# Kernel optimization log

Measured on AMD Instinct MI355X. Metric: run time of the kernel, lower is better.

The kernel has to match this reference:

```python
import jax, jax.numpy as jnp
import numpy as np

N = 50000
EPS = 1e-5


def gcn_conv(x, edge_index, W, b):
    # x: [N, Fin] -> [N, Fout]; symmetric-normalized aggregation with self-loops
    h = x @ W  # [N, Fout]
    src = jnp.concatenate([edge_index[0], jnp.arange(N, dtype=edge_index.dtype)])
    dst = jnp.concatenate([edge_index[1], jnp.arange(N, dtype=edge_index.dtype)])
    deg = jax.ops.segment_sum(jnp.ones_like(dst, dtype=h.dtype), dst, num_segments=N)
    dinv = jnp.where(deg > 0, jax.lax.rsqrt(deg), 0.0)
    norm = dinv[src] * dinv[dst]  # [E+N]
    msg = h[src] * norm[:, None]  # [E+N, Fout]
    out = jax.ops.segment_sum(msg, dst, num_segments=N)
    return out + b


def batch_norm_eval(x, gamma, beta, mean, var):
    return (x - mean) * jax.lax.rsqrt(var + EPS) * gamma + beta


def setup_inputs() -> dict:
    key = jax.random.key(0)
    ks = jax.random.split(key, 16)
    Fin, H, C = 128, 64, 40
    inp = {
        "x": jax.random.normal(ks[0], (N, Fin), dtype=jnp.float32),
        "edge_index": jax.random.randint(ks[1], (2, 1600000), 0, N, dtype=jnp.int64),
        "W1": jax.random.normal(ks[2], (Fin, H), dtype=jnp.float32) / np.sqrt(Fin),
        "b1": jnp.zeros((H,), jnp.float32),
        "g1": jax.random.normal(ks[3], (H,), jnp.float32) * 0.1 + 1.0,
        "be1": jax.random.normal(ks[4], (H,), jnp.float32) * 0.1,
        "m1": jax.random.normal(ks[5], (H,), jnp.float32) * 0.1,
        "v1": jax.random.uniform(ks[6], (H,), jnp.float32, 0.5, 1.5),
        "W2": jax.random.normal(ks[7], (H, H), dtype=jnp.float32) / np.sqrt(H),
        "b2": jnp.zeros((H,), jnp.float32),
        "g2": jax.random.normal(ks[8], (H,), jnp.float32) * 0.1 + 1.0,
        "be2": jax.random.normal(ks[9], (H,), jnp.float32) * 0.1,
        "m2": jax.random.normal(ks[10], (H,), jnp.float32) * 0.1,
        "v2": jax.random.uniform(ks[11], (H,), jnp.float32, 0.5, 1.5),
        "W3": jax.random.normal(ks[12], (H, C), dtype=jnp.float32) / np.sqrt(H),
        "b3": jnp.zeros((C,), jnp.float32),
    }
    return inp


def reference(x, edge_index, W1, b1, g1, be1, m1, v1, W2, b2, g2, be2, m2, v2, W3, b3):
    # eval-mode forward: dropout is identity, BatchNorm uses running stats
    h = gcn_conv(x, edge_index, W1, b1)
    h = jax.nn.relu(batch_norm_eval(h, g1, be1, m1, v1))
    h = gcn_conv(h, edge_index, W2, b2)
    h = jax.nn.relu(batch_norm_eval(h, g2, be2, m2, v2))
    return gcn_conv(h, edge_index, W3, b3)
```

## Files before the change

### kernel.cpp

```cpp
#include <hip/hip_runtime.h>
#include <hip/hip_fp16.h>

#define BN_EPS 1e-5f


__global__ void k_bcount(const int* __restrict__ dst, int* __restrict__ btot, int E, int B) {
    __shared__ int cnt[256];
    int tid = threadIdx.x;
    cnt[tid] = 0;
    __syncthreads();
    int e0 = blockIdx.x * 2048;
#pragma unroll
    for (int j = 0; j < 8; ++j) {
        int e = e0 + j * 256 + tid;
        if (e < E) atomicAdd(&cnt[dst[e] >> 8], 1);
    }
    __syncthreads();
    if (tid < B && cnt[tid] > 0) atomicAdd(&btot[tid], cnt[tid]);
}

__global__ void k_bscan(const int* __restrict__ btot, int* __restrict__ bbase,
                        int* __restrict__ bcur, int* __restrict__ row_ptr, int N, int B) {
    __shared__ int sc[256];
    int tid = threadIdx.x;
    int v = (tid < B) ? btot[tid] : 0;
    sc[tid] = v;
    __syncthreads();
    for (int off = 1; off < 256; off <<= 1) {
        int t = (tid >= off) ? sc[tid - off] : 0;
        __syncthreads();
        sc[tid] += t;
        __syncthreads();
    }
    int excl = sc[tid] - v;
    if (tid < B) { bbase[tid] = excl; bcur[tid] = excl; }
    if (tid == B - 1) { bbase[B] = excl + v; row_ptr[N] = excl + v; }
}

__global__ void k_bscatter(const int* __restrict__ src, const int* __restrict__ dst,
                           int* bcur, unsigned int* __restrict__ ebuf, int E, int B) {
    __shared__ int cnt[256];
    __shared__ int gb[256];
    int tid = threadIdx.x;
    cnt[tid] = 0;
    __syncthreads();
    int e0 = blockIdx.x * 2048;
    int bk[8], rk[8];
    unsigned int pay[8];
#pragma unroll
    for (int j = 0; j < 8; ++j) {
        int e = e0 + j * 256 + tid;
        if (e < E) {
            int d = dst[e];
            int b = d >> 8;
            bk[j] = b;
            rk[j] = atomicAdd(&cnt[b], 1);
            pay[j] = (unsigned int)src[e] | ((unsigned int)(d & 255) << 16);
        } else {
            bk[j] = -1; rk[j] = 0; pay[j] = 0;
        }
    }
    __syncthreads();
    if (tid < B && cnt[tid] > 0) gb[tid] = atomicAdd(&bcur[tid], cnt[tid]);
    __syncthreads();
#pragma unroll
    for (int j = 0; j < 8; ++j)
        if (bk[j] >= 0) ebuf[gb[bk[j]] + rk[j]] = pay[j];
}

__global__ void k_bfinal(const unsigned int* __restrict__ ebuf, const int* __restrict__ bbase,
                         int* __restrict__ row_ptr, float* __restrict__ dinv,
                         unsigned short* __restrict__ col, int N) {
    __shared__ int cnt[256];
    __shared__ int sc[256];
    __shared__ int cur[256];
    int tid = threadIdx.x;
    int b = blockIdx.x;
    int node0 = b << 8;
    int ebeg = bbase[b], eend = bbase[b + 1];

    cnt[tid] = 0;
    __syncthreads();
    for (int i = ebeg + tid; i < eend; i += 256)
        atomicAdd(&cnt[ebuf[i] >> 16], 1);
    __syncthreads();
    int myc = cnt[tid];
    sc[tid] = myc;
    __syncthreads();
    for (int off = 1; off < 256; off <<= 1) {
        int t = (tid >= off) ? sc[tid - off] : 0;
        __syncthreads();
        sc[tid] += t;
        __syncthreads();
    }
    int excl = sc[tid] - myc;
    cur[tid] = ebeg + excl;
    int node = node0 + tid;
    if (node < N) {
        row_ptr[node] = ebeg + excl;
        dinv[node] = rsqrtf((float)(myc + 1));
    }
    __syncthreads();
    for (int i = ebeg + tid; i < eend; i += 256) {
        unsigned int p = ebuf[i];
        int dl = p >> 16;
        int pos = atomicAdd(&cur[dl], 1);
        col[pos] = (unsigned short)(p & 0xFFFFu);
    }
}

template <int K, int FOUT>
__launch_bounds__(256)
__global__ void k_gemm_scale(const float* __restrict__ X, const float* __restrict__ W,
                             const float* __restrict__ dinv, __half* __restrict__ HS, int N) {
    __shared__ float xs[K][65];
    __shared__ float wl[K][FOUT];
    int tid = threadIdx.x;
    int row0 = blockIdx.x * 64;

    for (int idx = tid; idx < K * FOUT; idx += 256)
        wl[idx / FOUT][idx % FOUT] = W[idx];
    for (int idx = tid; idx < 64 * K; idx += 256) {
        int r = idx / K, k = idx % K;
        int row = row0 + r;
        xs[k][r] = (row < N) ? X[row * K + k] : 0.0f;
    }
    __syncthreads();

    int tc = tid & 15, tr = tid >> 4;
    if (4 * tc < FOUT) {
        float acc[4][4] = {};
#pragma unroll 8
        for (int k = 0; k < K; ++k) {
            float a0 = xs[k][4 * tr + 0];
            float a1 = xs[k][4 * tr + 1];
            float a2 = xs[k][4 * tr + 2];
            float a3 = xs[k][4 * tr + 3];
            const float4 w = *reinterpret_cast<const float4*>(&wl[k][4 * tc]);
            acc[0][0] += a0 * w.x; acc[0][1] += a0 * w.y; acc[0][2] += a0 * w.z; acc[0][3] += a0 * w.w;
            acc[1][0] += a1 * w.x; acc[1][1] += a1 * w.y; acc[1][2] += a1 * w.z; acc[1][3] += a1 * w.w;
            acc[2][0] += a2 * w.x; acc[2][1] += a2 * w.y; acc[2][2] += a2 * w.z; acc[2][3] += a2 * w.w;
            acc[3][0] += a3 * w.x; acc[3][1] += a3 * w.y; acc[3][2] += a3 * w.z; acc[3][3] += a3 * w.w;
        }
#pragma unroll
        for (int i = 0; i < 4; ++i) {
            int row = row0 + 4 * tr + i;
            if (row < N) {
                float dv = dinv[row];
                __half2 h0 = __floats2half2_rn(dv * acc[i][0], dv * acc[i][1]);
                __half2 h1 = __floats2half2_rn(dv * acc[i][2], dv * acc[i][3]);
                __half2* p = reinterpret_cast<__half2*>(&HS[row * FOUT + 4 * tc]);
                p[0] = h0; p[1] = h1;
            }
        }
    }
}

template <int FOUT, bool BN>
__launch_bounds__(256)
__global__ void k_agg(const __half2* __restrict__ hs2, const unsigned short* __restrict__ col,
                      const int* __restrict__ row_ptr, const float* __restrict__ dinv,
                      const float* __restrict__ b, const float* __restrict__ g,
                      const float* __restrict__ be, const float* __restrict__ m,
                      const float* __restrict__ v, float* __restrict__ out, int N) {
    constexpr int NP = FOUT / 2;
    int gtid = blockIdx.x * blockDim.x + threadIdx.x;
    int wave = gtid >> 6;
    int lane = gtid & 63;
    int half = lane >> 5;
    int l = lane & 31;
    int nwaves = (gridDim.x * blockDim.x) >> 6;
    bool active = l < NP;

    float b0 = 0.f, b1 = 0.f, s0f = 0.f, s1f = 0.f, t0f = 0.f, t1f = 0.f;
    if (active) {
        b0 = b[2 * l]; b1 = b[2 * l + 1];
        if (BN) {
            s0f = g[2 * l] * rsqrtf(v[2 * l] + BN_EPS);
            s1f = g[2 * l + 1] * rsqrtf(v[2 * l + 1] + BN_EPS);
            t0f = be[2 * l] - m[2 * l] * s0f;
            t1f = be[2 * l + 1] - m[2 * l + 1] * s1f;
        }
    }

    float2* out2 = reinterpret_cast<float2*>(out);

    for (int node = wave; node < N; node += nwaves) {
        int beg = row_ptr[node], end = row_ptr[node + 1];
        float ax = 0.f, ay = 0.f, bx = 0.f, by = 0.f;
        float cx = 0.f, cy = 0.f, dx = 0.f, dy = 0.f;
        if (active && half == 0) {
            float2 t = __half22float2(hs2[node * NP + l]);
            ax = t.x; ay = t.y;
        }
        int e = beg + half;
        for (; e + 6 < end; e += 8) {
            int i0 = col[e], i1 = col[e + 2], i2 = col[e + 4], i3 = col[e + 6];
            if (active) {
                float2 t0 = __half22float2(hs2[i0 * NP + l]);
                float2 t1 = __half22float2(hs2[i1 * NP + l]);
                float2 t2 = __half22float2(hs2[i2 * NP + l]);
                float2 t3 = __half22float2(hs2[i3 * NP + l]);
                ax += t0.x; ay += t0.y;
                bx += t1.x; by += t1.y;
                cx += t2.x; cy += t2.y;
                dx += t3.x; dy += t3.y;
            }
        }
        for (; e < end; e += 2) {
            int i0 = col[e];
            if (active) {
                float2 t0 = __half22float2(hs2[i0 * NP + l]);
                ax += t0.x; ay += t0.y;
            }
        }
        float sx = (ax + bx) + (cx + dx);
        float sy = (ay + by) + (cy + dy);
        sx += __shfl_xor(sx, 32);
        sy += __shfl_xor(sy, 32);
        if (active && half == 0) {
            float dv = dinv[node];
            float o0 = dv * sx + b0;
            float o1 = dv * sy + b1;
            if (BN) {
                o0 = fmaxf(o0 * s0f + t0f, 0.0f);
                o1 = fmaxf(o1 * s1f + t1f, 0.0f);
            }
            out2[node * NP + l] = make_float2(o0, o1);
        }
    }
}


extern "C" void kernel_launch(void* const* d_in, const int* in_sizes, int n_in,
                              void* d_out, int out_size, void* d_ws, size_t ws_size,
                              hipStream_t stream) {
    const float* x   = (const float*)d_in[0];
    const int*   ei  = (const int*)d_in[1];
    const float* W1  = (const float*)d_in[2];
    const float* b1  = (const float*)d_in[3];
    const float* g1  = (const float*)d_in[4];
    const float* be1 = (const float*)d_in[5];
    const float* m1  = (const float*)d_in[6];
    const float* v1  = (const float*)d_in[7];
    const float* W2  = (const float*)d_in[8];
    const float* b2  = (const float*)d_in[9];
    const float* g2  = (const float*)d_in[10];
    const float* be2 = (const float*)d_in[11];
    const float* m2  = (const float*)d_in[12];
    const float* v2  = (const float*)d_in[13];
    const float* W3  = (const float*)d_in[14];
    const float* b3  = (const float*)d_in[15];

    const int FIN = 128, H = 64;
    int N = in_sizes[0] / FIN;
    int E = in_sizes[1] / 2;
    const int* src = ei;
    const int* dst = ei + E;
    int B = (N + 255) >> 8;

    char* ws = (char*)d_ws;
    size_t off = 0;
    auto carve = [&](size_t bytes) -> void* {
        void* p = ws + off;
        off += (bytes + 255) & ~(size_t)255;
        return p;
    };
    float*  dinv    = (float*)carve((size_t)N * 4);
    int*    row_ptr = (int*)carve((size_t)(N + 1) * 4);
    unsigned short* col = (unsigned short*)carve((size_t)E * 2);
    unsigned int*   ebuf = (unsigned int*)carve((size_t)E * 4);
    __half* hs      = (__half*)carve((size_t)N * H * 2);
    float*  y       = (float*)carve((size_t)N * H * 4);
    int*    btot    = (int*)carve(512 * 4);
    int*    bbase   = (int*)carve(512 * 4);
    int*    bcur    = (int*)carve(512 * 4);
    (void)ws_size; (void)n_in; (void)out_size;

    int eb2k = (E + 2047) / 2048;

    hipMemsetAsync(btot, 0, (size_t)B * 4, stream);
    k_bcount<<<eb2k, 256, 0, stream>>>(dst, btot, E, B);
    k_bscan<<<1, 256, 0, stream>>>(btot, bbase, bcur, row_ptr, N, B);
    k_bscatter<<<eb2k, 256, 0, stream>>>(src, dst, bcur, ebuf, E, B);
    k_bfinal<<<B, 256, 0, stream>>>(ebuf, bbase, row_ptr, dinv, col, N);

    int gb = (N + 63) / 64;
    const __half2* hs2 = (const __half2*)hs;
    k_gemm_scale<128, 64><<<gb, 256, 0, stream>>>(x, W1, dinv, hs, N);
    k_agg<64, true><<<4096, 256, 0, stream>>>(hs2, col, row_ptr, dinv, b1, g1, be1, m1, v1, y, N);
    k_gemm_scale<64, 64><<<gb, 256, 0, stream>>>(y, W2, dinv, hs, N);
    k_agg<64, true><<<4096, 256, 0, stream>>>(hs2, col, row_ptr, dinv, b2, g2, be2, m2, v2, y, N);
    k_gemm_scale<64, 40><<<gb, 256, 0, stream>>>(y, W3, dinv, hs, N);
    k_agg<40, false><<<4096, 256, 0, stream>>>(hs2, col, row_ptr, dinv, b3, nullptr, nullptr, nullptr, nullptr,
                                               (float*)d_out, N);
}
```

Measured before the change: 262.5 us.

## Use fp16 dot2 in dense transforms and store intermediate activations in fp16

The GEMM kernels now stage inputs and weights in shared memory as packed half2 values and accumulate with the packed fp16 dot-product instruction into fp32, halving the multiply-add instruction count. The BN+ReLU aggregation outputs are written as fp16, and the following GEMMs read fp16 input with 16-byte loads, halving that intermediate traffic. The cost is extra rounding of the inputs, weights and hidden activations to fp16, which can reduce accuracy relative to the fp32 reference.

```diff
diff --git a/kernel.cpp b/kernel.cpp
--- a/kernel.cpp
+++ b/kernel.cpp
@@ -2,6 +2,13 @@
 #include <hip/hip_fp16.h>
 
 #define BN_EPS 1e-5f
+
+typedef _Float16 half2_t __attribute__((ext_vector_type(2)));
+typedef _Float16 half8_t __attribute__((ext_vector_type(8)));
+
+static __device__ __forceinline__ float fdot2(half2_t a, half2_t b, float c) {
+    return __builtin_amdgcn_fdot2(a, b, c, false);
+}
 
 
 __global__ void k_bcount(const int* __restrict__ dst, int* __restrict__ btot, int E, int B) {
@@ -109,48 +116,85 @@
     }
 }
 
-template <int K, int FOUT>
+template <int K, int FOUT, bool FP16IN>
 __launch_bounds__(256)
-__global__ void k_gemm_scale(const float* __restrict__ X, const float* __restrict__ W,
-                             const float* __restrict__ dinv, __half* __restrict__ HS, int N) {
-    __shared__ float xs[K][65];
-    __shared__ float wl[K][FOUT];
+__global__ void k_gemm_scale(const void* __restrict__ Xv, const float* __restrict__ W,
+                             const float* __restrict__ dinv, half2_t* __restrict__ HS, int N) {
+    constexpr int KK = K / 2;
+    constexpr int XSTR = (K == 128) ? 66 : 36;
+    __shared__ half2_t xs2[64][XSTR];
+    __shared__ half2_t wl2[KK][FOUT];
     int tid = threadIdx.x;
     int row0 = blockIdx.x * 64;
 
-    for (int idx = tid; idx < K * FOUT; idx += 256)
-        wl[idx / FOUT][idx % FOUT] = W[idx];
-    for (int idx = tid; idx < 64 * K; idx += 256) {
-        int r = idx / K, k = idx % K;
-        int row = row0 + r;
-        xs[k][r] = (row < N) ? X[row * K + k] : 0.0f;
+    if constexpr (FP16IN) {
+        const _Float16* X = (const _Float16*)Xv;
+        constexpr int U = 64 * K / 8;
+        for (int u = tid; u < U; u += 256) {
+            int row = u / (K / 8), q = u % (K / 8);
+            int grow = row0 + row;
+            uint4 v = make_uint4(0u, 0u, 0u, 0u);
+            if (grow < N) v = *(const uint4*)&X[(size_t)grow * K + q * 8];
+            *(uint4*)&xs2[row][q * 4] = v;
+        }
+    } else {
+        const float* X = (const float*)Xv;
+        constexpr int U = 64 * K / 4;
+        for (int u = tid; u < U; u += 256) {
+            int row = u / (K / 4), c = u % (K / 4);
+            int grow = row0 + row;
+            half2_t h0 = (half2_t)(_Float16)0, h1 = (half2_t)(_Float16)0;
+            if (grow < N) {
+                float4 v = *(const float4*)&X[(size_t)grow * K + c * 4];
+                h0[0] = (_Float16)v.x; h0[1] = (_Float16)v.y;
+                h1[0] = (_Float16)v.z; h1[1] = (_Float16)v.w;
+            }
+            xs2[row][2 * c] = h0;
+            xs2[row][2 * c + 1] = h1;
+        }
+    }
+    for (int i = tid; i < KK * FOUT; i += 256) {
+        int kk = i / FOUT, f = i % FOUT;
+        half2_t h;
+        h[0] = (_Float16)W[(2 * kk) * FOUT + f];
+        h[1] = (_Float16)W[(2 * kk + 1) * FOUT + f];
+        wl2[kk][f] = h;
     }
     __syncthreads();
 
     int tc = tid & 15, tr = tid >> 4;
     if (4 * tc < FOUT) {
         float acc[4][4] = {};
-#pragma unroll 8
-        for (int k = 0; k < K; ++k) {
-            float a0 = xs[k][4 * tr + 0];
-            float a1 = xs[k][4 * tr + 1];
-            float a2 = xs[k][4 * tr + 2];
-            float a3 = xs[k][4 * tr + 3];
-            const float4 w = *reinterpret_cast<const float4*>(&wl[k][4 * tc]);
-            acc[0][0] += a0 * w.x; acc[0][1] += a0 * w.y; acc[0][2] += a0 * w.z; acc[0][3] += a0 * w.w;
-            acc[1][0] += a1 * w.x; acc[1][1] += a1 * w.y; acc[1][2] += a1 * w.z; acc[1][3] += a1 * w.w;
-            acc[2][0] += a2 * w.x; acc[2][1] += a2 * w.y; acc[2][2] += a2 * w.z; acc[2][3] += a2 * w.w;
-            acc[3][0] += a3 * w.x; acc[3][1] += a3 * w.y; acc[3][2] += a3 * w.z; acc[3][3] += a3 * w.w;
+#pragma unroll 4
+        for (int kk = 0; kk < KK; ++kk) {
+            half2_t a0 = xs2[4 * tr + 0][kk];
+            half2_t a1 = xs2[4 * tr + 1][kk];
+            half2_t a2 = xs2[4 * tr + 2][kk];
+            half2_t a3 = xs2[4 * tr + 3][kk];
+            half8_t wv = *(const half8_t*)&wl2[kk][4 * tc];
+            half2_t w0 = {wv[0], wv[1]};
+            half2_t w1 = {wv[2], wv[3]};
+            half2_t w2 = {wv[4], wv[5]};
+            half2_t w3 = {wv[6], wv[7]};
+            acc[0][0] = fdot2(a0, w0, acc[0][0]); acc[0][1] = fdot2(a0, w1, acc[0][1]);
+            acc[0][2] = fdot2(a0, w2, acc[0][2]); acc[0][3] = fdot2(a0, w3, acc[0][3]);
+            acc[1][0] = fdot2(a1, w0, acc[1][0]); acc[1][1] = fdot2(a1, w1, acc[1][1]);
+            acc[1][2] = fdot2(a1, w2, acc[1][2]); acc[1][3] = fdot2(a1, w3, acc[1][3]);
+            acc[2][0] = fdot2(a2, w0, acc[2][0]); acc[2][1] = fdot2(a2, w1, acc[2][1]);
+            acc[2][2] = fdot2(a2, w2, acc[2][2]); acc[2][3] = fdot2(a2, w3, acc[2][3]);
+            acc[3][0] = fdot2(a3, w0, acc[3][0]); acc[3][1] = fdot2(a3, w1, acc[3][1]);
+            acc[3][2] = fdot2(a3, w2, acc[3][2]); acc[3][3] = fdot2(a3, w3, acc[3][3]);
         }
 #pragma unroll
         for (int i = 0; i < 4; ++i) {
             int row = row0 + 4 * tr + i;
             if (row < N) {
                 float dv = dinv[row];
-                __half2 h0 = __floats2half2_rn(dv * acc[i][0], dv * acc[i][1]);
-                __half2 h1 = __floats2half2_rn(dv * acc[i][2], dv * acc[i][3]);
-                __half2* p = reinterpret_cast<__half2*>(&HS[row * FOUT + 4 * tc]);
-                p[0] = h0; p[1] = h1;
+                half2_t p0, p1;
+                p0[0] = (_Float16)(dv * acc[i][0]); p0[1] = (_Float16)(dv * acc[i][1]);
+                p1[0] = (_Float16)(dv * acc[i][2]); p1[1] = (_Float16)(dv * acc[i][3]);
+                HS[(size_t)row * (FOUT / 2) + 2 * tc] = p0;
+                HS[(size_t)row * (FOUT / 2) + 2 * tc + 1] = p1;
             }
         }
     }
@@ -158,11 +202,11 @@
 
 template <int FOUT, bool BN>
 __launch_bounds__(256)
-__global__ void k_agg(const __half2* __restrict__ hs2, const unsigned short* __restrict__ col,
+__global__ void k_agg(const half2_t* __restrict__ hs2, const unsigned short* __restrict__ col,
                       const int* __restrict__ row_ptr, const float* __restrict__ dinv,
                       const float* __restrict__ b, const float* __restrict__ g,
                       const float* __restrict__ be, const float* __restrict__ m,
-                      const float* __restrict__ v, float* __restrict__ out, int N) {
+                      const float* __restrict__ v, void* __restrict__ outv, int N) {
     constexpr int NP = FOUT / 2;
     int gtid = blockIdx.x * blockDim.x + threadIdx.x;
     int wave = gtid >> 6;
@@ -183,35 +227,33 @@
         }
     }
 
-    float2* out2 = reinterpret_cast<float2*>(out);
-
     for (int node = wave; node < N; node += nwaves) {
         int beg = row_ptr[node], end = row_ptr[node + 1];
         float ax = 0.f, ay = 0.f, bx = 0.f, by = 0.f;
         float cx = 0.f, cy = 0.f, dx = 0.f, dy = 0.f;
         if (active && half == 0) {
-            float2 t = __half22float2(hs2[node * NP + l]);
-            ax = t.x; ay = t.y;
+            half2_t t = hs2[(size_t)node * NP + l];
+            ax = (float)t[0]; ay = (float)t[1];
         }
         int e = beg + half;
         for (; e + 6 < end; e += 8) {
             int i0 = col[e], i1 = col[e + 2], i2 = col[e + 4], i3 = col[e + 6];
             if (active) {
-                float2 t0 = __half22float2(hs2[i0 * NP + l]);
-                float2 t1 = __half22float2(hs2[i1 * NP + l]);
-                float2 t2 = __half22float2(hs2[i2 * NP + l]);
-                float2 t3 = __half22float2(hs2[i3 * NP + l]);
-                ax += t0.x; ay += t0.y;
-                bx += t1.x; by += t1.y;
-                cx += t2.x; cy += t2.y;
-                dx += t3.x; dy += t3.y;
+                half2_t t0 = hs2[(size_t)i0 * NP + l];
+                half2_t t1 = hs2[(size_t)i1 * NP + l];
+                half2_t t2 = hs2[(size_t)i2 * NP + l];
+                half2_t t3 = hs2[(size_t)i3 * NP + l];
+                ax += (float)t0[0]; ay += (float)t0[1];
+                bx += (float)t1[0]; by += (float)t1[1];
+                cx += (float)t2[0]; cy += (float)t2[1];
+                dx += (float)t3[0]; dy += (float)t3[1];
             }
         }
         for (; e < end; e += 2) {
             int i0 = col[e];
             if (active) {
-                float2 t0 = __half22float2(hs2[i0 * NP + l]);
-                ax += t0.x; ay += t0.y;
+                half2_t t0 = hs2[(size_t)i0 * NP + l];
+                ax += (float)t0[0]; ay += (float)t0[1];
             }
         }
         float sx = (ax + bx) + (cx + dx);
@@ -225,8 +267,12 @@
             if (BN) {
                 o0 = fmaxf(o0 * s0f + t0f, 0.0f);
                 o1 = fmaxf(o1 * s1f + t1f, 0.0f);
-            }
-            out2[node * NP + l] = make_float2(o0, o1);
+                half2_t h;
+                h[0] = (_Float16)o0; h[1] = (_Float16)o1;
+                ((half2_t*)outv)[(size_t)node * NP + l] = h;
+            } else {
+                ((float2*)outv)[(size_t)node * NP + l] = make_float2(o0, o1);
+            }
         }
     }
 }
@@ -270,8 +316,8 @@
     int*    row_ptr = (int*)carve((size_t)(N + 1) * 4);
     unsigned short* col = (unsigned short*)carve((size_t)E * 2);
     unsigned int*   ebuf = (unsigned int*)carve((size_t)E * 4);
-    __half* hs      = (__half*)carve((size_t)N * H * 2);
-    float*  y       = (float*)carve((size_t)N * H * 4);
+    half2_t* hs     = (half2_t*)carve((size_t)N * H * 2);
+    _Float16* y     = (_Float16*)carve((size_t)N * H * 2);
     int*    btot    = (int*)carve(512 * 4);
     int*    bbase   = (int*)carve(512 * 4);
     int*    bcur    = (int*)carve(512 * 4);
@@ -286,12 +332,11 @@
     k_bfinal<<<B, 256, 0, stream>>>(ebuf, bbase, row_ptr, dinv, col, N);
 
     int gb = (N + 63) / 64;
-    const __half2* hs2 = (const __half2*)hs;
-    k_gemm_scale<128, 64><<<gb, 256, 0, stream>>>(x, W1, dinv, hs, N);
-    k_agg<64, true><<<4096, 256, 0, stream>>>(hs2, col, row_ptr, dinv, b1, g1, be1, m1, v1, y, N);
-    k_gemm_scale<64, 64><<<gb, 256, 0, stream>>>(y, W2, dinv, hs, N);
-    k_agg<64, true><<<4096, 256, 0, stream>>>(hs2, col, row_ptr, dinv, b2, g2, be2, m2, v2, y, N);
-    k_gemm_scale<64, 40><<<gb, 256, 0, stream>>>(y, W3, dinv, hs, N);
-    k_agg<40, false><<<4096, 256, 0, stream>>>(hs2, col, row_ptr, dinv, b3, nullptr, nullptr, nullptr, nullptr,
-                                               (float*)d_out, N);
-}
+    k_gemm_scale<128, 64, false><<<gb, 256, 0, stream>>>(x, W1, dinv, hs, N);
+    k_agg<64, true><<<4096, 256, 0, stream>>>(hs, col, row_ptr, dinv, b1, g1, be1, m1, v1, y, N);
+    k_gemm_scale<64, 64, true><<<gb, 256, 0, stream>>>(y, W2, dinv, hs, N);
+    k_agg<64, true><<<4096, 256, 0, stream>>>(hs, col, row_ptr, dinv, b2, g2, be2, m2, v2, y, N);
+    k_gemm_scale<64, 40, true><<<gb, 256, 0, stream>>>(y, W3, dinv, hs, N);
+    k_agg<40, false><<<4096, 256, 0, stream>>>(hs, col, row_ptr, dinv, b3, nullptr, nullptr, nullptr, nullptr,
+                                               d_out, N);
+}
```

New measurement: 235.6 us. -10.3%, faster.
